# Performance work log

Measured on AMD Instinct MI355X. Metric: run time of the kernel, lower is better.

The kernel has to match this reference:

```python
import jax, jax.numpy as jnp
from jax import lax
import numpy as np

B, N, C_IN = 2, 16384, 64
NPOINT, NSAMPLE = 4096, 32
RADIUS = 0.5


def setup_inputs() -> dict:
    key = jax.random.key(0)
    ks = jax.random.split(key, 8)
    xyz = jax.random.normal(ks[0], (B, N, 3), jnp.float32)
    features = jax.random.normal(ks[1], (B, C_IN, N), jnp.float32)

    def lin(k, o, i):
        return jax.random.normal(k, (o, i), jnp.float32) * (1.0 / np.sqrt(i))

    w1 = lin(ks[2], 64, C_IN + 3); b1 = jnp.zeros((64,), jnp.float32)
    w2 = lin(ks[3], 64, 64);       b2 = jnp.zeros((64,), jnp.float32)
    w3 = lin(ks[4], 128, 64);      b3 = jnp.zeros((128,), jnp.float32)
    wa = lin(ks[5], 128, 128);     ba = jnp.zeros((128,), jnp.float32)
    wc = lin(ks[6], 1, 128);       bc = jnp.zeros((1,), jnp.float32)
    return dict(xyz=xyz, features=features, w1=w1, b1=b1, w2=w2, b2=b2,
                w3=w3, b3=b3, wa=wa, ba=ba, wc=wc, bc=bc)


def farthest_point_sample(xyz, npoint):
    # d-fps: iterative furthest point sampling, seeded at index 0 (CUDA semantics)
    Bn, Nn, _ = xyz.shape

    def body(carry, _):
        dist, far = carry                                   # (B,N), (B,)
        centroid = jnp.take_along_axis(xyz, far[:, None, None], axis=1)  # (B,1,3)
        d = jnp.sum((xyz - centroid) ** 2, axis=-1)          # (B,N)
        dist = jnp.minimum(dist, d)
        nxt = jnp.argmax(dist, axis=-1).astype(jnp.int32)
        return (dist, nxt), far

    dist0 = jnp.full((Bn, Nn), 1e10, xyz.dtype)
    far0 = jnp.zeros((Bn,), jnp.int32)
    _, idx = lax.scan(body, (dist0, far0), None, length=npoint)
    return idx.T  # (B, npoint)


def ball_query(xyz, new_xyz, radius, nsample):
    # first-nsample-within-radius semantics of pointnet2 ball_query
    Nn = xyz.shape[1]
    d2 = jnp.sum((new_xyz[:, :, None, :] - xyz[:, None, :, :]) ** 2, axis=-1)  # (B,S,N)
    mask = d2 < radius * radius
    keys = jnp.where(mask, jnp.arange(Nn, dtype=jnp.int32), Nn)
    negv, _ = lax.top_k(-keys, nsample)      # nsample smallest in-ball indices
    idx = -negv                              # (B,S,nsample)
    idx_cnt = jnp.sum(mask, axis=-1)         # (B,S)
    valid = idx < Nn
    idx = jnp.where(valid, idx, idx[..., :1])          # pad with first valid idx
    idx = jnp.where(idx_cnt[..., None] > 0, idx, 0)    # empty balls -> 0 (masked later)
    return idx_cnt, idx


def reference(xyz, features, w1, b1, w2, b2, w3, b3, wa, ba, wc, bc):
    bidx = jnp.arange(B)[:, None, None]
    # sampling (d-fps) + gather
    sample_idx = farthest_point_sample(xyz, NPOINT)                    # (B,S)
    new_xyz = jnp.take_along_axis(xyz, sample_idx[..., None], axis=1)  # (B,S,3)
    # grouping (QueryAndGroup, use_xyz=True)
    idx_cnt, idx = ball_query(xyz, new_xyz, RADIUS, NSAMPLE)
    grouped_xyz = xyz[bidx, idx] - new_xyz[:, :, None, :]              # (B,S,ns,3)
    feats_t = jnp.swapaxes(features, 1, 2)                             # (B,N,C)
    grouped_feat = feats_t[bidx, idx]                                  # (B,S,ns,C)
    h = jnp.concatenate([grouped_xyz, grouped_feat], axis=-1)          # (B,S,ns,3+C)
    # shared MLP (1x1 conv + ReLU stack)
    h = jax.nn.relu(jnp.einsum('bsni,oi->bsno', h, w1) + b1)
    h = jax.nn.relu(jnp.einsum('bsni,oi->bsno', h, w2) + b2)
    h = jax.nn.relu(jnp.einsum('bsni,oi->bsno', h, w3) + b3)
    # zero empty-ball groups, then max-pool over neighbors
    h = h * (idx_cnt > 0)[:, :, None, None].astype(h.dtype)
    pooled = jnp.max(h, axis=2)                                        # (B,S,128)
    # aggregation mlp (1x1 conv1d + ReLU)
    agg = jax.nn.relu(jnp.einsum('bsi,oi->bso', pooled, wa) + ba)      # (B,S,128)
    # confidence mlp -> (B,S)
    scores = (jnp.einsum('bsi,oi->bso', agg, wc) + bc)[..., 0]
    new_features = jnp.swapaxes(agg, 1, 2)                             # (B,128,S)
    return new_xyz, new_features, scores
```

## Files before the change

### kernel.cpp

```cpp
#include <hip/hip_runtime.h>
#include <cstddef>

constexpr int kB = 2;
constexpr int kN = 16384;
constexpr int kC = 64;
constexpr int kS = 4096;
constexpr int kNS = 32;
constexpr int kNC16 = 1024;

__device__ __forceinline__ unsigned expand10(unsigned v) {
  v &= 1023u;
  v = (v | (v << 16)) & 0x030000FFu;
  v = (v | (v <<  8)) & 0x0300F00Fu;
  v = (v | (v <<  4)) & 0x030C30C3u;
  v = (v | (v <<  2)) & 0x09249249u;
  return v;
}

template <int C>
__device__ __forceinline__ unsigned dpp_u32(unsigned x) {
  return (unsigned)__builtin_amdgcn_update_dpp((int)x, (int)x, C, 0xF, 0xF, false);
}
__device__ __forceinline__ unsigned rowmax16(unsigned x) {
  x = max(x, dpp_u32<0x121>(x));
  x = max(x, dpp_u32<0x122>(x));
  x = max(x, dpp_u32<0x124>(x));
  x = max(x, dpp_u32<0x128>(x));
  return x;
}
template <int C>
__device__ __forceinline__ void u64max_dpp(unsigned& hi, unsigned& lo) {
  unsigned h2 = dpp_u32<C>(hi), l2 = dpp_u32<C>(lo);
  bool g = (h2 > hi) || (h2 == hi && l2 > lo);
  hi = g ? h2 : hi;
  lo = g ? l2 : lo;
}

__global__ void transpose_kernel(const float* __restrict__ in,
                                 float* __restrict__ out,
                                 int Cdim, int Ndim) {
  __shared__ float tile[32][33];
  int b = blockIdx.z;
  int n0 = blockIdx.x * 32;
  int c0 = blockIdx.y * 32;
  int tx = threadIdx.x;
  const float* inb = in + (size_t)b * Cdim * Ndim;
  float* outb = out + (size_t)b * Cdim * Ndim;
#pragma unroll
  for (int i = threadIdx.y; i < 32; i += 8)
    tile[i][tx] = inb[(size_t)(c0 + i) * Ndim + (n0 + tx)];
  __syncthreads();
#pragma unroll
  for (int i = threadIdx.y; i < 32; i += 8)
    outb[(size_t)(n0 + i) * Cdim + (c0 + tx)] = tile[tx][i];
}

__global__ __launch_bounds__(1024) void fps_prep_kernel(
    const float* __restrict__ xyz, float4* __restrict__ pxyz,
    float* __restrict__ ctr, float* __restrict__ rad) {
  const int b = blockIdx.x;
  const int t = threadIdx.x;
  const int lane = t & 63;
  const int w = t >> 6;
  const float* P = xyz + (size_t)b * kN * 3;
  __shared__ unsigned long long keys[kN];
  __shared__ float sbb[6][16];

  float mnx = 3e38f, mny = 3e38f, mnz = 3e38f;
  float mxx = -3e38f, mxy = -3e38f, mxz = -3e38f;
  for (int p = t; p < kN; p += 1024) {
    float x = P[p * 3], y = P[p * 3 + 1], z = P[p * 3 + 2];
    mnx = fminf(mnx, x); mny = fminf(mny, y); mnz = fminf(mnz, z);
    mxx = fmaxf(mxx, x); mxy = fmaxf(mxy, y); mxz = fmaxf(mxz, z);
  }
#pragma unroll
  for (int off = 32; off >= 1; off >>= 1) {
    mnx = fminf(mnx, __shfl_xor(mnx, off, 64));
    mny = fminf(mny, __shfl_xor(mny, off, 64));
    mnz = fminf(mnz, __shfl_xor(mnz, off, 64));
    mxx = fmaxf(mxx, __shfl_xor(mxx, off, 64));
    mxy = fmaxf(mxy, __shfl_xor(mxy, off, 64));
    mxz = fmaxf(mxz, __shfl_xor(mxz, off, 64));
  }
  if (lane == 0) {
    sbb[0][w] = mnx; sbb[1][w] = mny; sbb[2][w] = mnz;
    sbb[3][w] = mxx; sbb[4][w] = mxy; sbb[5][w] = mxz;
  }
  __syncthreads();
  mnx = sbb[0][lane & 15]; mny = sbb[1][lane & 15]; mnz = sbb[2][lane & 15];
  mxx = sbb[3][lane & 15]; mxy = sbb[4][lane & 15]; mxz = sbb[5][lane & 15];
#pragma unroll
  for (int off = 8; off >= 1; off >>= 1) {
    mnx = fminf(mnx, __shfl_xor(mnx, off, 64));
    mny = fminf(mny, __shfl_xor(mny, off, 64));
    mnz = fminf(mnz, __shfl_xor(mnz, off, 64));
    mxx = fmaxf(mxx, __shfl_xor(mxx, off, 64));
    mxy = fmaxf(mxy, __shfl_xor(mxy, off, 64));
    mxz = fmaxf(mxz, __shfl_xor(mxz, off, 64));
  }
  __syncthreads();
  const float sx = 1023.0f / fmaxf(mxx - mnx, 1e-20f);
  const float sy = 1023.0f / fmaxf(mxy - mny, 1e-20f);
  const float sz = 1023.0f / fmaxf(mxz - mnz, 1e-20f);
  for (int p = t; p < kN; p += 1024) {
    float x = P[p * 3], y = P[p * 3 + 1], z = P[p * 3 + 2];
    int qx = (int)((x - mnx) * sx); qx = max(0, min(1023, qx));
    int qy = (int)((y - mny) * sy); qy = max(0, min(1023, qy));
    int qz = (int)((z - mnz) * sz); qz = max(0, min(1023, qz));
    unsigned mort = (expand10((unsigned)qx) << 2) |
                    (expand10((unsigned)qy) << 1) | expand10((unsigned)qz);
    keys[p] = ((unsigned long long)mort << 14) | (unsigned)p;
  }
  __syncthreads();
  for (unsigned k = 2; k <= (unsigned)kN; k <<= 1) {
    for (unsigned j = k >> 1; j > 0; j >>= 1) {
      for (int i = t; i < kN; i += 1024) {
        int l = i ^ (int)j;
        if (l > i) {
          unsigned long long a = keys[i], c = keys[l];
          bool asc = ((i & (int)k) == 0);
          if ((a > c) == asc) { keys[i] = c; keys[l] = a; }
        }
      }
      __syncthreads();
    }
  }
  float4* PX = pxyz + (size_t)b * kN;
  for (int i = t; i < kN; i += 1024) {
    int o = (int)(keys[i] & 0x3FFFull);
    PX[i] = float4{P[o * 3], P[o * 3 + 1], P[o * 3 + 2], __int_as_float(o)};
  }
  if (t < kNC16) {
    float amn = 3e38f, bmn = 3e38f, cmn = 3e38f;
    float amx = -3e38f, bmx = -3e38f, cmx = -3e38f;
    for (int kk = 0; kk < 16; kk++) {
      int o = (int)(keys[t * 16 + kk] & 0x3FFFull);
      float x = P[o * 3], y = P[o * 3 + 1], z = P[o * 3 + 2];
      amn = fminf(amn, x); amx = fmaxf(amx, x);
      bmn = fminf(bmn, y); bmx = fmaxf(bmx, y);
      cmn = fminf(cmn, z); cmx = fmaxf(cmx, z);
    }
    float ux = (amn + amx) * 0.5f, uy = (bmn + bmx) * 0.5f, uz = (cmn + cmx) * 0.5f;
    float hx = (amx - amn) * 0.5f, hy = (bmx - bmn) * 0.5f, hz = (cmx - cmn) * 0.5f;
    float r = sqrtf(hx * hx + hy * hy + hz * hz) * 1.0002f + 1e-6f;
    ctr[((size_t)b * kNC16 + t) * 3 + 0] = ux;
    ctr[((size_t)b * kNC16 + t) * 3 + 1] = uy;
    ctr[((size_t)b * kNC16 + t) * 3 + 2] = uz;
    rad[(size_t)b * kNC16 + t] = r;
  }
}

__global__ __launch_bounds__(1024) void fps_kernel(
    const float* __restrict__ xyz, const float4* __restrict__ pxyz,
    const float* __restrict__ ctr, const float* __restrict__ rad,
    float* __restrict__ new_xyz) {
  const int b = blockIdx.x;
  const int t = threadIdx.x;
  const int lane = t & 63;
  const int w = t >> 6;
  const int g = lane >> 4;
  const int sub = lane & 15;
  const int poff = (w << 4) | sub;
  const int s0 = (w << 6) | lane;
  const float* P = xyz + (size_t)b * kN * 3;
  const float4* PX = pxyz + (size_t)b * kN;

  __shared__ float dist[kN];
  __shared__ unsigned Mhi[kNC16], Mlo[kNC16];
  __shared__ float cux[kNC16], cuy[kNC16], cuz[kNC16], crd[kNC16];
  __shared__ unsigned whi[2][16], wlo[2][16];

  for (int i = t; i < kN; i += 1024) dist[i] = 1e10f;
  if (t < kNC16) {
    const int c = t;
    const int s = ((c & 15) << 6) | (c >> 4);
    cux[s] = ctr[((size_t)b * kNC16 + c) * 3 + 0];
    cuy[s] = ctr[((size_t)b * kNC16 + c) * 3 + 1];
    cuz[s] = ctr[((size_t)b * kNC16 + c) * 3 + 2];
    crd[s] = rad[(size_t)b * kNC16 + c];
    Mhi[s] = __float_as_uint(1e10f);
    Mlo[s] = 16383u;
  }
  __syncthreads();

  float cx = P[0], cy = P[1], cz = P[2];

  for (int it = 0; it < kS; ++it) {
    if (t == 0) {
      float* o = new_xyz + ((size_t)b * kS + it) * 3;
      o[0] = cx; o[1] = cy; o[2] = cz;
    }
    {
      float dxu = cx - cux[s0], dyu = cy - cuy[s0], dzu = cz - cuz[s0];
      float du = sqrtf(dxu * dxu + dyu * dyu + dzu * dzu);
      float lb = du - crd[s0] - 1e-5f;
      float Mv = __uint_as_float(Mhi[s0]);
      bool fail = !((lb > 0.0f) && (lb * lb >= Mv * 1.00001f));
      unsigned long long fmask = __ballot(fail);
      while (fmask) {
        int b0 = (int)__ffsll(fmask) - 1; fmask &= fmask - 1;
        int b1 = fmask ? (int)__ffsll(fmask) - 1 : b0; if (fmask) fmask &= fmask - 1;
        int b2 = fmask ? (int)__ffsll(fmask) - 1 : b0; if (fmask) fmask &= fmask - 1;
        int b3 = fmask ? (int)__ffsll(fmask) - 1 : b0; if (fmask) fmask &= fmask - 1;
        int bA = (g & 1) ? b1 : b0;
        int bBq = (g & 1) ? b3 : b2;
        int bg = (g & 2) ? bBq : bA;
        int p = (bg << 8) | poff;
        float4 v = PX[p];
        float dold = dist[p];
        float ddx = cx - v.x, ddy = cy - v.y, ddz = cz - v.z;
        float d = __fadd_rn(__fadd_rn(__fmul_rn(ddx, ddx), __fmul_rn(ddy, ddy)),
                            __fmul_rn(ddz, ddz));
        float dk = fminf(dold, d);
        dist[p] = dk;
        unsigned fb = __float_as_uint(dk);
        unsigned mx = rowmax16(fb);
        unsigned sel = (fb == mx) ? (16383u - (unsigned)__float_as_int(v.w)) : 0u;
        unsigned m2 = rowmax16(sel);
        if (sub == 0) {
          int sl = (w << 6) | bg;
          Mhi[sl] = mx;
          Mlo[sl] = m2;
        }
      }
    }
    {
      unsigned hi = Mhi[s0], lo = Mlo[s0];
      u64max_dpp<0xB1>(hi, lo);
      u64max_dpp<0x4E>(hi, lo);
      u64max_dpp<0x124>(hi, lo);
      u64max_dpp<0x128>(hi, lo);
      u64max_dpp<0x142>(hi, lo);
      u64max_dpp<0x143>(hi, lo);
      if (lane == 63) { whi[it & 1][w] = hi; wlo[it & 1][w] = lo; }
    }
    __syncthreads();
    {
      unsigned hi = whi[it & 1][sub], lo = wlo[it & 1][sub];
      u64max_dpp<0x121>(hi, lo);
      u64max_dpp<0x122>(hi, lo);
      u64max_dpp<0x124>(hi, lo);
      u64max_dpp<0x128>(hi, lo);
      int orig = 16383 - (int)(lo & 0x3FFFu);
      cx = P[orig * 3];
      cy = P[orig * 3 + 1];
      cz = P[orig * 3 + 2];
    }
  }
}

__global__ __launch_bounds__(256) void ball_query_kernel(const float* __restrict__ xyz,
                                                         const float* __restrict__ new_xyz,
                                                         int* __restrict__ idx) {
  const int q = (int)((blockIdx.x * 256 + threadIdx.x) >> 6);
  const int lane = threadIdx.x & 63;
  const int b = q >> 12;
  const float* P = xyz + (size_t)b * kN * 3;
  const float qx = new_xyz[q * 3 + 0];
  const float qy = new_xyz[q * 3 + 1];
  const float qz = new_xyz[q * 3 + 2];
  int cnt = 0;
  int first = -1;
  const int base = q * kNS;
  for (int j = 0; j < kN / 64; j++) {
    const int p = (j << 6) + lane;
    float dx = P[p * 3 + 0] - qx;
    float dy = P[p * 3 + 1] - qy;
    float dz = P[p * 3 + 2] - qz;
    float d = __fadd_rn(__fadd_rn(__fmul_rn(dx, dx), __fmul_rn(dy, dy)),
                        __fmul_rn(dz, dz));
    bool inb = d < 0.25f;
    unsigned long long m = __ballot(inb);
    if (first < 0 && m != 0ull) first = (j << 6) + (__ffsll(m) - 1);
    if (inb && cnt < kNS) {
      int r = cnt + (int)__popcll(m & ((1ull << lane) - 1ull));
      if (r < kNS) idx[base + r] = p;
    }
    cnt += (int)__popcll(m);
    if (cnt >= kNS) break;
  }
  if (cnt < kNS) {
    int fill = (first >= 0) ? first : 0;
    if (lane >= cnt && lane < kNS) idx[base + lane] = fill;
  }
}

__global__ __launch_bounds__(128) void group_mlp_kernel(
    const float* __restrict__ xyz, const float* __restrict__ new_xyz,
    const float* __restrict__ featsT, const int* __restrict__ nidx,
    const float* __restrict__ w1, const float* __restrict__ b1,
    const float* __restrict__ w2, const float* __restrict__ b2,
    const float* __restrict__ w3, const float* __restrict__ b3,
    const float* __restrict__ wa, const float* __restrict__ ba,
    const float* __restrict__ wc, const float* __restrict__ bc,
    float* __restrict__ aggT, float* __restrict__ scores) {
  __shared__ float smem[2 * 4384];
  const int wid = threadIdx.x >> 6;
  const int lane = threadIdx.x & 63;
  const int q = blockIdx.x * 2 + wid;
  const int b = q >> 12;
  float* Xs = smem + wid * 4384;
  float* H1 = Xs + 32 * 68;
  float* pool = H1 + 32 * 64;
  int* idxs = (int*)(pool + 128);

  if (lane < 32) idxs[lane] = nidx[q * kNS + lane];
  const float qx = new_xyz[q * 3 + 0];
  const float qy = new_xyz[q * 3 + 1];
  const float qz = new_xyz[q * 3 + 2];
  __syncthreads();

  const float* P = xyz + (size_t)b * kN * 3;
  const float* F = featsT + (size_t)b * kN * kC;
  if (lane < 32) {
    int p = idxs[lane];
    Xs[lane * 68 + 0] = P[p * 3 + 0] - qx;
    Xs[lane * 68 + 1] = P[p * 3 + 1] - qy;
    Xs[lane * 68 + 2] = P[p * 3 + 2] - qz;
  } else {
    Xs[(lane - 32) * 68 + 67] = 0.0f;
  }
  for (int j = 0; j < 32; j++) {
    Xs[j * 68 + 3 + lane] = F[(size_t)idxs[j] * kC + lane];
  }
  __syncthreads();

  float w[68];
  {
    const int o = lane;
#pragma unroll
    for (int k = 0; k < 67; k++) w[k] = w1[o * 67 + k];
    w[67] = 0.0f;
    const float bias = b1[o];
    for (int r = 0; r < 32; r++) {
      float acc = bias;
#pragma unroll
      for (int k4 = 0; k4 < 17; k4++) {
        float4 x = *(const float4*)&Xs[r * 68 + k4 * 4];
        acc += x.x * w[k4 * 4 + 0] + x.y * w[k4 * 4 + 1] +
               x.z * w[k4 * 4 + 2] + x.w * w[k4 * 4 + 3];
      }
      H1[r * 64 + o] = fmaxf(acc, 0.0f);
    }
  }
  __syncthreads();
  {
    const int o = lane;
#pragma unroll
    for (int k = 0; k < 64; k++) w[k] = w2[o * 64 + k];
    const float bias = b2[o];
    for (int r = 0; r < 32; r++) {
      float acc = bias;
#pragma unroll
      for (int k4 = 0; k4 < 16; k4++) {
        float4 x = *(const float4*)&H1[r * 64 + k4 * 4];
        acc += x.x * w[k4 * 4 + 0] + x.y * w[k4 * 4 + 1] +
               x.z * w[k4 * 4 + 2] + x.w * w[k4 * 4 + 3];
      }
      Xs[r * 64 + o] = fmaxf(acc, 0.0f);
    }
  }
  __syncthreads();
  {
    const int c = lane;
    float wB[64];
#pragma unroll
    for (int k = 0; k < 64; k++) {
      w[k] = w3[c * 64 + k];
      wB[k] = w3[(c + 64) * 64 + k];
    }
    const float biasA = b3[c];
    const float biasB = b3[c + 64];
    float pa = 0.0f, pb = 0.0f;
    for (int r = 0; r < 32; r++) {
      float a = biasA, bb = biasB;
#pragma unroll
      for (int k4 = 0; k4 < 16; k4++) {
        float4 x = *(const float4*)&Xs[r * 64 + k4 * 4];
        a  += x.x * w[k4 * 4 + 0] + x.y * w[k4 * 4 + 1] +
              x.z * w[k4 * 4 + 2] + x.w * w[k4 * 4 + 3];
        bb += x.x * wB[k4 * 4 + 0] + x.y * wB[k4 * 4 + 1] +
              x.z * wB[k4 * 4 + 2] + x.w * wB[k4 * 4 + 3];
      }
      pa = fmaxf(pa, a);
      pb = fmaxf(pb, bb);
    }
    pool[c] = pa;
    pool[c + 64] = pb;
  }
  __syncthreads();
  {
    const int c = lane;
    float accA = ba[c], accB = ba[c + 64];
#pragma unroll
    for (int k4 = 0; k4 < 32; k4++) {
      float4 pv = *(const float4*)&pool[k4 * 4];
      float4 wva = *(const float4*)&wa[c * 128 + k4 * 4];
      float4 wvb = *(const float4*)&wa[(c + 64) * 128 + k4 * 4];
      accA += pv.x * wva.x + pv.y * wva.y + pv.z * wva.z + pv.w * wva.w;
      accB += pv.x * wvb.x + pv.y * wvb.y + pv.z * wvb.z + pv.w * wvb.w;
    }
    float aggA = fmaxf(accA, 0.0f);
    float aggB = fmaxf(accB, 0.0f);
    aggT[(size_t)q * 128 + c] = aggA;
    aggT[(size_t)q * 128 + 64 + c] = aggB;
    float partial = aggA * wc[c] + aggB * wc[c + 64];
#pragma unroll
    for (int off = 32; off >= 1; off >>= 1) partial += __shfl_xor(partial, off, 64);
    if (lane == 0) scores[q] = partial + bc[0];
  }
}

extern "C" void kernel_launch(void* const* d_in, const int* in_sizes, int n_in,
                              void* d_out, int out_size, void* d_ws, size_t ws_size,
                              hipStream_t stream) {
  const float* xyz   = (const float*)d_in[0];
  const float* feats = (const float*)d_in[1];
  const float* w1 = (const float*)d_in[2];
  const float* b1 = (const float*)d_in[3];
  const float* w2 = (const float*)d_in[4];
  const float* b2 = (const float*)d_in[5];
  const float* w3 = (const float*)d_in[6];
  const float* b3 = (const float*)d_in[7];
  const float* wa = (const float*)d_in[8];
  const float* ba = (const float*)d_in[9];
  const float* wc = (const float*)d_in[10];
  const float* bc = (const float*)d_in[11];

  float* out_new_xyz = (float*)d_out;
  float* out_feat    = out_new_xyz + (size_t)kB * kS * 3;
  float* out_scores  = out_feat + (size_t)kB * 128 * kS;

  char* ws = (char*)d_ws;
  float* featsT = (float*)ws;
  int*   idxbuf = (int*)(ws + (size_t)8 * 1024 * 1024);
  float* aggT   = (float*)(ws + (size_t)9 * 1024 * 1024);
  float4* pxyzb = (float4*)(ws + (size_t)9 * 1024 * 1024);
  float* ctrb   = (float*)(ws + (size_t)9 * 1024 * 1024 + 512 * 1024);
  float* radb   = (float*)(ws + (size_t)9 * 1024 * 1024 + 544 * 1024);

  transpose_kernel<<<dim3(kN / 32, kC / 32, kB), dim3(32, 8, 1), 0, stream>>>(
      feats, featsT, kC, kN);
  fps_prep_kernel<<<dim3(kB), dim3(1024), 0, stream>>>(
      xyz, pxyzb, ctrb, radb);
  fps_kernel<<<dim3(kB), dim3(1024), 0, stream>>>(
      xyz, pxyzb, ctrb, radb, out_new_xyz);
  ball_query_kernel<<<dim3(kB * kS / 4), dim3(256), 0, stream>>>(
      xyz, out_new_xyz, idxbuf);
  group_mlp_kernel<<<dim3(kB * kS / 2), dim3(128), 0, stream>>>(
      xyz, out_new_xyz, featsT, idxbuf,
      w1, b1, w2, b2, w3, b3, wa, ba, wc, bc, aggT, out_scores);
  transpose_kernel<<<dim3(128 / 32, kS / 32, kB), dim3(32, 8, 1), 0, stream>>>(
      aggT, out_feat, kS, 128);
}
```

Measured before the change: 6.389 ms.

## Restructure FPS cluster pruning with AABB bounds, SoA packed math and compacted lists

The FPS kernel now prunes Morton clusters with a box-distance lower bound, which is tighter than the previous bounding-sphere test. Cluster bounds are held in registers instead of shared memory. Point data is stored as structure-of-arrays pairs so packed v_pk_add/v_pk_mul compute two distances per lane. Failing clusters are compacted into a per-wave list and processed eight per pass with 8-lane reductions, replacing the four-at-a-time ffs loop. The aim is to cut per-iteration latency in the serial 4096-step loop, at the cost of inline asm, more complex indexing and a workspace layout that must match.

```diff
diff --git a/kernel.cpp b/kernel.cpp
--- a/kernel.cpp
+++ b/kernel.cpp
@@ -7,6 +7,9 @@
 constexpr int kS = 4096;
 constexpr int kNS = 32;
 constexpr int kNC16 = 1024;
+constexpr int kNP = kN / 2;
+
+typedef float f32x2 __attribute__((ext_vector_type(2)));
 
 __device__ __forceinline__ unsigned expand10(unsigned v) {
   v &= 1023u;
@@ -21,11 +24,10 @@
 __device__ __forceinline__ unsigned dpp_u32(unsigned x) {
   return (unsigned)__builtin_amdgcn_update_dpp((int)x, (int)x, C, 0xF, 0xF, false);
 }
-__device__ __forceinline__ unsigned rowmax16(unsigned x) {
-  x = max(x, dpp_u32<0x121>(x));
-  x = max(x, dpp_u32<0x122>(x));
-  x = max(x, dpp_u32<0x124>(x));
-  x = max(x, dpp_u32<0x128>(x));
+__device__ __forceinline__ unsigned max8(unsigned x) {
+  x = max(x, dpp_u32<0xB1>(x));
+  x = max(x, dpp_u32<0x4E>(x));
+  x = max(x, dpp_u32<0x141>(x));
   return x;
 }
 template <int C>
@@ -35,6 +37,9 @@
   hi = g ? h2 : hi;
   lo = g ? l2 : lo;
 }
+
+#define PK_ADD(d, a, b) asm("v_pk_add_f32 %0, %1, %2" : "=v"(d) : "v"(a), "v"(b))
+#define PK_MUL(d, a, b) asm("v_pk_mul_f32 %0, %1, %2" : "=v"(d) : "v"(a), "v"(b))
 
 __global__ void transpose_kernel(const float* __restrict__ in,
                                  float* __restrict__ out,
@@ -56,8 +61,9 @@
 }
 
 __global__ __launch_bounds__(1024) void fps_prep_kernel(
-    const float* __restrict__ xyz, float4* __restrict__ pxyz,
-    float* __restrict__ ctr, float* __restrict__ rad) {
+    const float* __restrict__ xyz, float* __restrict__ pxx,
+    float* __restrict__ pxy, float* __restrict__ pxz,
+    unsigned* __restrict__ pxo, float* __restrict__ aabb) {
   const int b = blockIdx.x;
   const int t = threadIdx.x;
   const int lane = t & 63;
@@ -125,10 +131,18 @@
       __syncthreads();
     }
   }
-  float4* PX = pxyz + (size_t)b * kN;
+  float* FX = pxx + (size_t)b * kN;
+  float* FY = pxy + (size_t)b * kN;
+  float* FZ = pxz + (size_t)b * kN;
+  unsigned* FO = pxo + (size_t)b * kN;
   for (int i = t; i < kN; i += 1024) {
     int o = (int)(keys[i] & 0x3FFFull);
-    PX[i] = float4{P[o * 3], P[o * 3 + 1], P[o * 3 + 2], __int_as_float(o)};
+    int c = i >> 4, j = i & 15;
+    int fi = c * 16 + ((j & 7) << 1) + (j >> 3);
+    FX[fi] = P[o * 3];
+    FY[fi] = P[o * 3 + 1];
+    FZ[fi] = P[o * 3 + 2];
+    FO[fi] = 16383u - (unsigned)o;
   }
   if (t < kNC16) {
     float amn = 3e38f, bmn = 3e38f, cmn = 3e38f;
@@ -140,47 +154,47 @@
       bmn = fminf(bmn, y); bmx = fmaxf(bmx, y);
       cmn = fminf(cmn, z); cmx = fmaxf(cmx, z);
     }
-    float ux = (amn + amx) * 0.5f, uy = (bmn + bmx) * 0.5f, uz = (cmn + cmx) * 0.5f;
-    float hx = (amx - amn) * 0.5f, hy = (bmx - bmn) * 0.5f, hz = (cmx - cmn) * 0.5f;
-    float r = sqrtf(hx * hx + hy * hy + hz * hz) * 1.0002f + 1e-6f;
-    ctr[((size_t)b * kNC16 + t) * 3 + 0] = ux;
-    ctr[((size_t)b * kNC16 + t) * 3 + 1] = uy;
-    ctr[((size_t)b * kNC16 + t) * 3 + 2] = uz;
-    rad[(size_t)b * kNC16 + t] = r;
+    float* AB = aabb + (size_t)b * 6 * kNC16;
+    AB[0 * kNC16 + t] = (amn + amx) * 0.5f;
+    AB[1 * kNC16 + t] = (bmn + bmx) * 0.5f;
+    AB[2 * kNC16 + t] = (cmn + cmx) * 0.5f;
+    AB[3 * kNC16 + t] = (amx - amn) * 0.5f * 1.0001f + 2e-7f;
+    AB[4 * kNC16 + t] = (bmx - bmn) * 0.5f * 1.0001f + 2e-7f;
+    AB[5 * kNC16 + t] = (cmx - cmn) * 0.5f * 1.0001f + 2e-7f;
   }
 }
 
 __global__ __launch_bounds__(1024) void fps_kernel(
-    const float* __restrict__ xyz, const float4* __restrict__ pxyz,
-    const float* __restrict__ ctr, const float* __restrict__ rad,
-    float* __restrict__ new_xyz) {
+    const float* __restrict__ xyz,
+    const float* __restrict__ pxx, const float* __restrict__ pxy,
+    const float* __restrict__ pxz, const unsigned* __restrict__ pxo,
+    const float* __restrict__ aabb, float* __restrict__ new_xyz) {
   const int b = blockIdx.x;
   const int t = threadIdx.x;
   const int lane = t & 63;
   const int w = t >> 6;
-  const int g = lane >> 4;
-  const int sub = lane & 15;
-  const int poff = (w << 4) | sub;
+  const int grp = lane >> 3;
+  const int sub8 = lane & 7;
   const int s0 = (w << 6) | lane;
   const float* P = xyz + (size_t)b * kN * 3;
-  const float4* PX = pxyz + (size_t)b * kN;
-
-  __shared__ float dist[kN];
-  __shared__ unsigned Mhi[kNC16], Mlo[kNC16];
-  __shared__ float cux[kNC16], cuy[kNC16], cuz[kNC16], crd[kNC16];
+  const f32x2* XP = (const f32x2*)(pxx + (size_t)b * kN);
+  const f32x2* YP = (const f32x2*)(pxy + (size_t)b * kN);
+  const f32x2* ZP = (const f32x2*)(pxz + (size_t)b * kN);
+  const uint2* OP = (const uint2*)(pxo + (size_t)b * kN);
+
+  __shared__ f32x2 dpair[kNP];
+  __shared__ uint2 M2[kNC16];
+  __shared__ unsigned list_[16][64];
   __shared__ unsigned whi[2][16], wlo[2][16];
 
-  for (int i = t; i < kN; i += 1024) dist[i] = 1e10f;
-  if (t < kNC16) {
-    const int c = t;
-    const int s = ((c & 15) << 6) | (c >> 4);
-    cux[s] = ctr[((size_t)b * kNC16 + c) * 3 + 0];
-    cuy[s] = ctr[((size_t)b * kNC16 + c) * 3 + 1];
-    cuz[s] = ctr[((size_t)b * kNC16 + c) * 3 + 2];
-    crd[s] = rad[(size_t)b * kNC16 + c];
-    Mhi[s] = __float_as_uint(1e10f);
-    Mlo[s] = 16383u;
-  }
+  for (int i = t; i < kNP; i += 1024) dpair[i] = f32x2{1e10f, 1e10f};
+  if (t < kNC16) M2[t] = uint2{__float_as_uint(1e10f), 0u};
+
+  const int c0 = (lane << 4) | w;
+  const float* AB = aabb + (size_t)b * 6 * kNC16;
+  float ux = AB[c0], uy = AB[kNC16 + c0], uz = AB[2 * kNC16 + c0];
+  float hx = AB[3 * kNC16 + c0], hy = AB[4 * kNC16 + c0], hz = AB[5 * kNC16 + c0];
+  asm volatile("" : "+v"(ux), "+v"(uy), "+v"(uz), "+v"(hx), "+v"(hy), "+v"(hz));
   __syncthreads();
 
   float cx = P[0], cy = P[1], cz = P[2];
@@ -191,41 +205,53 @@
       o[0] = cx; o[1] = cy; o[2] = cz;
     }
     {
-      float dxu = cx - cux[s0], dyu = cy - cuy[s0], dzu = cz - cuz[s0];
-      float du = sqrtf(dxu * dxu + dyu * dyu + dzu * dzu);
-      float lb = du - crd[s0] - 1e-5f;
-      float Mv = __uint_as_float(Mhi[s0]);
-      bool fail = !((lb > 0.0f) && (lb * lb >= Mv * 1.00001f));
+      float txd = fmaxf(fabsf(cx - ux) - hx, 0.0f);
+      float tyd = fmaxf(fabsf(cy - uy) - hy, 0.0f);
+      float tzd = fmaxf(fabsf(cz - uz) - hz, 0.0f);
+      float lb2 = txd * txd + tyd * tyd + tzd * tzd;
+      float Mv = __uint_as_float(M2[s0].x);
+      bool fail = !(lb2 >= Mv * 1.00001f + 1e-5f);
       unsigned long long fmask = __ballot(fail);
-      while (fmask) {
-        int b0 = (int)__ffsll(fmask) - 1; fmask &= fmask - 1;
-        int b1 = fmask ? (int)__ffsll(fmask) - 1 : b0; if (fmask) fmask &= fmask - 1;
-        int b2 = fmask ? (int)__ffsll(fmask) - 1 : b0; if (fmask) fmask &= fmask - 1;
-        int b3 = fmask ? (int)__ffsll(fmask) - 1 : b0; if (fmask) fmask &= fmask - 1;
-        int bA = (g & 1) ? b1 : b0;
-        int bBq = (g & 1) ? b3 : b2;
-        int bg = (g & 2) ? bBq : bA;
-        int p = (bg << 8) | poff;
-        float4 v = PX[p];
-        float dold = dist[p];
-        float ddx = cx - v.x, ddy = cy - v.y, ddz = cz - v.z;
-        float d = __fadd_rn(__fadd_rn(__fmul_rn(ddx, ddx), __fmul_rn(ddy, ddy)),
-                            __fmul_rn(ddz, ddz));
-        float dk = fminf(dold, d);
-        dist[p] = dk;
-        unsigned fb = __float_as_uint(dk);
-        unsigned mx = rowmax16(fb);
-        unsigned sel = (fb == mx) ? (16383u - (unsigned)__float_as_int(v.w)) : 0u;
-        unsigned m2 = rowmax16(sel);
-        if (sub == 0) {
-          int sl = (w << 6) | bg;
-          Mhi[sl] = mx;
-          Mlo[sl] = m2;
-        }
+      int nf = (int)__popcll(fmask);
+      if (fail) {
+        int pos = (int)__popcll(fmask & ((1ull << lane) - 1ull));
+        list_[w][pos] = (unsigned)lane;
+      }
+      const f32x2 ncx = f32x2{-cx, -cx};
+      const f32x2 ncy = f32x2{-cy, -cy};
+      const f32x2 ncz = f32x2{-cz, -cz};
+      const int npass = (nf + 7) >> 3;
+      for (int i = 0; i < npass; ++i) {
+        int idx = min(i * 8 + grp, nf - 1);
+        int cl = (int)list_[w][idx];
+        int pb = (((cl << 4) | w) << 3) | sub8;
+        f32x2 xp = XP[pb], yp = YP[pb], zp = ZP[pb];
+        uint2 op = OP[pb];
+        f32x2 dold = dpair[pb];
+        f32x2 dx_, dy_, dz_, xx_, yy_, zz_, s1_, d2_;
+        PK_ADD(dx_, xp, ncx);
+        PK_ADD(dy_, yp, ncy);
+        PK_ADD(dz_, zp, ncz);
+        PK_MUL(xx_, dx_, dx_);
+        PK_MUL(yy_, dy_, dy_);
+        PK_MUL(zz_, dz_, dz_);
+        PK_ADD(s1_, xx_, yy_);
+        PK_ADD(d2_, s1_, zz_);
+        f32x2 dk;
+        dk.x = fminf(dold.x, d2_.x);
+        dk.y = fminf(dold.y, d2_.y);
+        dpair[pb] = dk;
+        unsigned fa = __float_as_uint(dk.x), fbv = __float_as_uint(dk.y);
+        unsigned mx = max8(max(fa, fbv));
+        unsigned sa = (fa == mx) ? op.x : 0u;
+        unsigned sb = (fbv == mx) ? op.y : 0u;
+        unsigned m2v = max8(max(sa, sb));
+        if (sub8 == 0) M2[(w << 6) | cl] = uint2{mx, m2v};
       }
     }
     {
-      unsigned hi = Mhi[s0], lo = Mlo[s0];
+      uint2 m = M2[s0];
+      unsigned hi = m.x, lo = m.y;
       u64max_dpp<0xB1>(hi, lo);
       u64max_dpp<0x4E>(hi, lo);
       u64max_dpp<0x124>(hi, lo);
@@ -236,7 +262,7 @@
     }
     __syncthreads();
     {
-      unsigned hi = whi[it & 1][sub], lo = wlo[it & 1][sub];
+      unsigned hi = whi[it & 1][lane & 15], lo = wlo[it & 1][lane & 15];
       u64max_dpp<0x121>(hi, lo);
       u64max_dpp<0x122>(hi, lo);
       u64max_dpp<0x124>(hi, lo);
@@ -435,16 +461,18 @@
   float* featsT = (float*)ws;
   int*   idxbuf = (int*)(ws + (size_t)8 * 1024 * 1024);
   float* aggT   = (float*)(ws + (size_t)9 * 1024 * 1024);
-  float4* pxyzb = (float4*)(ws + (size_t)9 * 1024 * 1024);
-  float* ctrb   = (float*)(ws + (size_t)9 * 1024 * 1024 + 512 * 1024);
-  float* radb   = (float*)(ws + (size_t)9 * 1024 * 1024 + 544 * 1024);
+  float*    pxx = (float*)(ws + (size_t)9 * 1024 * 1024);
+  float*    pxy = (float*)(ws + (size_t)9 * 1024 * 1024 + 128 * 1024);
+  float*    pxz = (float*)(ws + (size_t)9 * 1024 * 1024 + 256 * 1024);
+  unsigned* pxo = (unsigned*)(ws + (size_t)9 * 1024 * 1024 + 384 * 1024);
+  float*   aabb = (float*)(ws + (size_t)9 * 1024 * 1024 + 512 * 1024);
 
   transpose_kernel<<<dim3(kN / 32, kC / 32, kB), dim3(32, 8, 1), 0, stream>>>(
       feats, featsT, kC, kN);
   fps_prep_kernel<<<dim3(kB), dim3(1024), 0, stream>>>(
-      xyz, pxyzb, ctrb, radb);
+      xyz, pxx, pxy, pxz, pxo, aabb);
   fps_kernel<<<dim3(kB), dim3(1024), 0, stream>>>(
-      xyz, pxyzb, ctrb, radb, out_new_xyz);
+      xyz, pxx, pxy, pxz, pxo, aabb, out_new_xyz);
   ball_query_kernel<<<dim3(kB * kS / 4), dim3(256), 0, stream>>>(
       xyz, out_new_xyz, idxbuf);
   group_mlp_kernel<<<dim3(kB * kS / 2), dim3(128), 0, stream>>>(
```

After: 6.175 ms. 1.03x faster.
